# Performance work log

Measured on AMD Instinct MI355X. Metric: run time of the kernel, lower is better.

## Reference

```python
import jax, jax.numpy as jnp
import numpy as np

B, L, H, T, C = 64, 1024, 512, 100, 97


def setup_inputs() -> dict:
    key = jax.random.key(0)
    k1, k2, k3, k4, k5 = jax.random.split(key, 5)
    return {
        "position_fmap": jax.random.normal(k1, (B, L, H), dtype=jnp.float32),
        "origin_fmap": jax.random.normal(k2, (B, L, H), dtype=jnp.float32),
        "pos_emb": jax.random.normal(k3, (T, H), dtype=jnp.float32),
        "W_gen": jax.random.normal(k4, (C, H), dtype=jnp.float32) * (1.0 / np.sqrt(H)),
        "b_gen": jax.random.normal(k5, (C,), dtype=jnp.float32) * 0.01,
    }


def reference(position_fmap, origin_fmap, pos_emb, W_gen, b_gen):
    # The torch loop over t in [0, T) computes, per step, scores = fmap @ emb_t,
    # softmax over L, then context = a^T @ origin_fmap. Batched over all steps:
    scores = jnp.einsum('blh,th->btl', position_fmap, pos_emb)   # [B, T, L]
    attn = jax.nn.softmax(scores, axis=-1)                       # softmax over spatial L
    context = jnp.einsum('btl,blh->bth', attn, origin_fmap)      # [B, T, H]
    # generator: Linear(H -> num_classes)
    return jnp.einsum('bth,ch->btc', context, W_gen) + b_gen     # [B, T, C]
```

## Files before the change

### kernel.cpp

```cpp
#include <hip/hip_runtime.h>
#include <hip/hip_bf16.h>

#define B_   64
#define L_   1024
#define H_   512
#define T_   100
#define C_   97
#define TP_  112

typedef _Float16 h8 __attribute__((ext_vector_type(8)));
typedef __attribute__((ext_vector_type(4))) float f32x4;

__global__ __launch_bounds__(256) void k0_prep(
    const float* __restrict__ emb, const float* __restrict__ W,
    _Float16* __restrict__ embh, _Float16* __restrict__ Wh) {
  const int row = blockIdx.x, tid = threadIdx.x;
  if (row < TP_) {
    for (int j = tid; j < H_; j += 256)
      embh[(size_t)row * H_ + j] =
          (row < T_) ? (_Float16)emb[(size_t)row * H_ + j] : (_Float16)0.f;
  } else {
    const int c = row - TP_;
    for (int j = tid; j < H_; j += 256)
      Wh[(size_t)c * H_ + j] =
          (c < C_) ? (_Float16)W[(size_t)c * H_ + j] : (_Float16)0.f;
  }
}

__global__ __launch_bounds__(256, 4) void k1_scores(
    const float* __restrict__ fmap, const _Float16* __restrict__ embh,
    _Float16* __restrict__ scT, float* __restrict__ part) {
  __shared__ float red_m[4 * TP_];
  __shared__ float red_s[4 * TP_];
  __shared__ float sMb[TP_];
  __shared__ _Float16 tile[TP_ * 72];
  const int tid = threadIdx.x;
  const int wave = tid >> 6, lane = tid & 63;
  const int quad = lane >> 4, cc = lane & 15;
  const int b = blockIdx.x >> 4;
  const int m0 = blockIdx.x * 64 + wave * 16;

  f32x4 acc[7];
#pragma unroll
  for (int i = 0; i < 7; ++i) acc[i] = (f32x4){0.f, 0.f, 0.f, 0.f};

  const float* ap = fmap + (size_t)(m0 + cc) * H_ + quad * 8;
#pragma unroll 2
  for (int k = 0; k < H_; k += 32) {
    float4 x0 = *(const float4*)(ap + k);
    float4 x1 = *(const float4*)(ap + k + 4);
    h8 a;
    a[0] = (_Float16)x0.x; a[1] = (_Float16)x0.y;
    a[2] = (_Float16)x0.z; a[3] = (_Float16)x0.w;
    a[4] = (_Float16)x1.x; a[5] = (_Float16)x1.y;
    a[6] = (_Float16)x1.z; a[7] = (_Float16)x1.w;
#pragma unroll
    for (int i = 0; i < 7; ++i) {
      h8 bf = *(const h8*)(embh + (size_t)(i * 16 + cc) * H_ + k + quad * 8);
      acc[i] = __builtin_amdgcn_mfma_f32_16x16x32_f16(a, bf, acc[i], 0, 0, 0);
    }
  }

  float pm[7], ps[7];
#pragma unroll
  for (int i = 0; i < 7; ++i) {
    float m = acc[i][0];
#pragma unroll
    for (int r = 1; r < 4; ++r) m = fmaxf(m, acc[i][r]);
    float s = 0.f;
#pragma unroll
    for (int r = 0; r < 4; ++r) s += __expf(acc[i][r] - m);
    pm[i] = m; ps[i] = s;
  }
#pragma unroll
  for (int d = 16; d < 64; d <<= 1) {
#pragma unroll
    for (int i = 0; i < 7; ++i) {
      float om = __shfl_xor(pm[i], d, 64);
      float os = __shfl_xor(ps[i], d, 64);
      float M = fmaxf(pm[i], om);
      ps[i] = ps[i] * __expf(pm[i] - M) + os * __expf(om - M);
      pm[i] = M;
    }
  }
  if (lane < 16) {
#pragma unroll
    for (int i = 0; i < 7; ++i) {
      red_m[wave * TP_ + i * 16 + lane] = pm[i];
      red_s[wave * TP_ + i * 16 + lane] = ps[i];
    }
  }
  __syncthreads();
  if (tid < TP_) {
    float M = red_m[tid], S = red_s[tid];
#pragma unroll
    for (int w = 1; w < 4; ++w) {
      float om = red_m[w * TP_ + tid], os = red_s[w * TP_ + tid];
      float nM = fmaxf(M, om);
      S = S * __expf(M - nM) + os * __expf(om - nM);
      M = nM;
    }
    float* p = part + ((size_t)blockIdx.x * TP_ + tid) * 2;
    p[0] = M; p[1] = S;
    sMb[tid] = M;
  }
  __syncthreads();
#pragma unroll
  for (int i = 0; i < 7; ++i) {
    float mb = sMb[i * 16 + cc];
#pragma unroll
    for (int r = 0; r < 4; ++r)
      tile[(i * 16 + cc) * 72 + wave * 16 + quad * 4 + r] = (_Float16)(acc[i][r] - mb);
  }
  __syncthreads();
  _Float16* dst = scT + (size_t)b * TP_ * L_ + (size_t)(blockIdx.x & 15) * 64;
  for (int idx = tid; idx < 896; idx += 256) {
    const int t = idx >> 3, c = idx & 7;
    h8 v = *(const h8*)&tile[t * 72 + c * 8];
    *(h8*)(dst + (size_t)t * L_ + c * 8) = v;
  }
}

__global__ __launch_bounds__(256) void k2_softmax(
    const _Float16* __restrict__ scT, const float* __restrict__ part,
    _Float16* __restrict__ attnT) {
  __shared__ float sAdj[16 * 14];
  __shared__ float sInv[14];
  const int b = blockIdx.x >> 3, tg = blockIdx.x & 7;
  const int tid = threadIdx.x;
  if (tid < 14) {
    const int t = tg * 14 + tid;
    float M = -1e30f, S = 0.f;
    for (int k = 0; k < 16; ++k) {
      const float* p = part + ((size_t)(b * 16 + k) * TP_ + t) * 2;
      float om = p[0], os = p[1];
      float nM = fmaxf(M, om);
      S = S * __expf(M - nM) + os * __expf(om - nM);
      M = nM;
    }
    sInv[tid] = 1.f / S;
    for (int k = 0; k < 16; ++k)
      sAdj[k * 14 + tid] = part[((size_t)(b * 16 + k) * TP_ + t) * 2] - M;
  }
  __syncthreads();
  const size_t base = ((size_t)b * TP_ + tg * 14) * L_;
  for (int idx = tid; idx < 14 * 128; idx += 256) {
    const int t = idx >> 7, c = idx & 127;
    const size_t off = base + (size_t)t * L_ + c * 8;
    h8 v = *(const h8*)(scT + off);
    const float adj = sAdj[(c >> 3) * 14 + t];
    const float inv = sInv[t];
    h8 o;
#pragma unroll
    for (int j = 0; j < 8; ++j)
      o[j] = (_Float16)(__expf((float)v[j] + adj) * inv);
    *(h8*)(attnT + off) = o;
  }
}

__global__ __launch_bounds__(256) void k3_context(
    const _Float16* __restrict__ attnT, const float* __restrict__ origin,
    _Float16* __restrict__ ctx) {
  const int b = blockIdx.x >> 3, hb = (blockIdx.x & 7) * 64;
  const int tid = threadIdx.x;
  const int wave = tid >> 6, lane = tid & 63;
  const int quad = lane >> 4, cc = lane & 15;

  f32x4 acc[7];
#pragma unroll
  for (int i = 0; i < 7; ++i) acc[i] = (f32x4){0.f, 0.f, 0.f, 0.f};

  const _Float16* aA = attnT + ((size_t)b * TP_ + cc) * L_ + quad * 8;
  const float* bp = origin + ((size_t)b * L_ + quad * 8) * H_ + hb + wave * 16 + cc;

#pragma unroll 2
  for (int l0 = 0; l0 < L_; l0 += 32) {
    h8 bfh;
#pragma unroll
    for (int j = 0; j < 8; ++j) bfh[j] = (_Float16)bp[(size_t)(l0 + j) * H_];
#pragma unroll
    for (int i = 0; i < 7; ++i) {
      h8 af = *(const h8*)(aA + (size_t)(i * 16) * L_ + l0);
      acc[i] = __builtin_amdgcn_mfma_f32_16x16x32_f16(af, bfh, acc[i], 0, 0, 0);
    }
  }
  const int h = hb + wave * 16 + cc;
#pragma unroll
  for (int i = 0; i < 7; ++i)
#pragma unroll
    for (int r = 0; r < 4; ++r)
      ctx[((size_t)b * TP_ + i * 16 + quad * 4 + r) * H_ + h] = (_Float16)acc[i][r];
}

__global__ __launch_bounds__(256) void k4_out(
    const _Float16* __restrict__ ctx, const _Float16* __restrict__ Wh,
    const float* __restrict__ bias, float* __restrict__ out) {
  const int b = blockIdx.x / 7, mt = blockIdx.x % 7;
  const int tid = threadIdx.x;
  const int wave = tid >> 6, lane = tid & 63;
  const int quad = lane >> 4, cc = lane & 15;
  f32x4 acc0 = (f32x4){0.f, 0.f, 0.f, 0.f};
  f32x4 acc1 = (f32x4){0.f, 0.f, 0.f, 0.f};
  const int c0 = wave * 16 + cc;
  const int c1 = (wave + 4) * 16 + cc;
  const bool hasB = (wave < 3);
  const _Float16* ap  = ctx + ((size_t)b * TP_ + mt * 16 + cc) * H_ + quad * 8;
  const _Float16* b0p = Wh + (size_t)c0 * H_ + quad * 8;
  const _Float16* b1p = Wh + (size_t)(hasB ? c1 : c0) * H_ + quad * 8;
#pragma unroll 2
  for (int k = 0; k < H_; k += 32) {
    h8 af = *(const h8*)(ap + k);
    h8 bf0 = *(const h8*)(b0p + k);
    acc0 = __builtin_amdgcn_mfma_f32_16x16x32_f16(af, bf0, acc0, 0, 0, 0);
    if (hasB) {
      h8 bf1 = *(const h8*)(b1p + k);
      acc1 = __builtin_amdgcn_mfma_f32_16x16x32_f16(af, bf1, acc1, 0, 0, 0);
    }
  }
  const float bias0 = (c0 < C_) ? bias[c0] : 0.f;
  const float bias1 = (hasB && c1 < C_) ? bias[c1] : 0.f;
#pragma unroll
  for (int r = 0; r < 4; ++r) {
    const int t = mt * 16 + quad * 4 + r;
    if (t < T_) {
      if (c0 < C_) out[((size_t)b * T_ + t) * C_ + c0] = acc0[r] + bias0;
      if (hasB && c1 < C_) out[((size_t)b * T_ + t) * C_ + c1] = acc1[r] + bias1;
    }
  }
}

extern "C" void kernel_launch(void* const* d_in, const int* in_sizes, int n_in,
                              void* d_out, int out_size, void* d_ws, size_t ws_size,
                              hipStream_t stream) {
  const float* fmap   = (const float*)d_in[0];
  const float* origin = (const float*)d_in[1];
  const float* emb    = (const float*)d_in[2];
  const float* W      = (const float*)d_in[3];
  const float* bias   = (const float*)d_in[4];
  float* out = (float*)d_out;

  char* ws = (char*)d_ws;
  _Float16* embh  = (_Float16*)(ws);
  _Float16* Wh    = (_Float16*)(ws + 114688);
  _Float16* scT   = (_Float16*)(ws + 229376);
  float*    part  = (float*)   (ws + 14909440);
  _Float16* attnT = (_Float16*)(ws + 15826944);
  _Float16* ctx   = (_Float16*)(ws + 30507008);

  hipLaunchKernelGGL(k0_prep,    dim3(224),  dim3(256), 0, stream, emb, W, embh, Wh);
  hipLaunchKernelGGL(k1_scores,  dim3(1024), dim3(256), 0, stream, fmap, embh, scT, part);
  hipLaunchKernelGGL(k2_softmax, dim3(512),  dim3(256), 0, stream, scT, part, attnT);
  hipLaunchKernelGGL(k3_context, dim3(512),  dim3(256), 0, stream, attnT, origin, ctx);
  hipLaunchKernelGGL(k4_out,     dim3(448),  dim3(256), 0, stream, ctx, Wh, bias, out);
}
```

Measured before the change: 375.7 us.

## Split context GEMM over L, move score transpose into softmax, widen score blocks

The context kernel gains a 4-way split over the sequence dimension, going from 512 to 2048 blocks and writing four partial fp16 context buffers. The output kernel sums those partials before its GEMM. The scores kernel now uses 512-thread blocks covering 128 rows and writes untransposed scores straight to global memory. The softmax kernel transposes them through shared memory. The intent is better occupancy and parallelism in the heavy context GEMM, at the cost of extra partial-buffer traffic, fp16 partial-sum precision loss, and uncoalesced strided score stores.

```diff
diff --git a/kernel.cpp b/kernel.cpp
--- a/kernel.cpp
+++ b/kernel.cpp
@@ -27,25 +27,23 @@
   }
 }
 
-__global__ __launch_bounds__(256, 4) void k1_scores(
+__global__ __launch_bounds__(512, 4) void k1_scores(
     const float* __restrict__ fmap, const _Float16* __restrict__ embh,
-    _Float16* __restrict__ scT, float* __restrict__ part) {
-  __shared__ float red_m[4 * TP_];
-  __shared__ float red_s[4 * TP_];
+    _Float16* __restrict__ sc, float* __restrict__ part) {
+  __shared__ float red_m[8 * TP_];
+  __shared__ float red_s[8 * TP_];
   __shared__ float sMb[TP_];
-  __shared__ _Float16 tile[TP_ * 72];
   const int tid = threadIdx.x;
   const int wave = tid >> 6, lane = tid & 63;
   const int quad = lane >> 4, cc = lane & 15;
-  const int b = blockIdx.x >> 4;
-  const int m0 = blockIdx.x * 64 + wave * 16;
+  const int m0 = blockIdx.x * 128 + wave * 16;
 
   f32x4 acc[7];
 #pragma unroll
   for (int i = 0; i < 7; ++i) acc[i] = (f32x4){0.f, 0.f, 0.f, 0.f};
 
   const float* ap = fmap + (size_t)(m0 + cc) * H_ + quad * 8;
-#pragma unroll 2
+#pragma unroll 4
   for (int k = 0; k < H_; k += 32) {
     float4 x0 = *(const float4*)(ap + k);
     float4 x1 = *(const float4*)(ap + k + 4);
@@ -94,7 +92,7 @@
   if (tid < TP_) {
     float M = red_m[tid], S = red_s[tid];
 #pragma unroll
-    for (int w = 1; w < 4; ++w) {
+    for (int w = 1; w < 8; ++w) {
       float om = red_m[w * TP_ + tid], os = red_s[w * TP_ + tid];
       float nM = fmaxf(M, om);
       S = S * __expf(M - nM) + os * __expf(om - nM);
@@ -110,58 +108,60 @@
     float mb = sMb[i * 16 + cc];
 #pragma unroll
     for (int r = 0; r < 4; ++r)
-      tile[(i * 16 + cc) * 72 + wave * 16 + quad * 4 + r] = (_Float16)(acc[i][r] - mb);
-  }
-  __syncthreads();
-  _Float16* dst = scT + (size_t)b * TP_ * L_ + (size_t)(blockIdx.x & 15) * 64;
-  for (int idx = tid; idx < 896; idx += 256) {
-    const int t = idx >> 3, c = idx & 7;
-    h8 v = *(const h8*)&tile[t * 72 + c * 8];
-    *(h8*)(dst + (size_t)t * L_ + c * 8) = v;
+      sc[(size_t)(m0 + quad * 4 + r) * TP_ + i * 16 + cc] =
+          (_Float16)(acc[i][r] - mb);
   }
 }
 
 __global__ __launch_bounds__(256) void k2_softmax(
-    const _Float16* __restrict__ scT, const float* __restrict__ part,
+    const _Float16* __restrict__ sc, const float* __restrict__ part,
     _Float16* __restrict__ attnT) {
-  __shared__ float sAdj[16 * 14];
-  __shared__ float sInv[14];
-  const int b = blockIdx.x >> 3, tg = blockIdx.x & 7;
-  const int tid = threadIdx.x;
-  if (tid < 14) {
-    const int t = tg * 14 + tid;
+  __shared__ float sAdj[TP_], sInv[TP_];
+  __shared__ _Float16 tile[TP_ * 152];
+  const int b = blockIdx.x >> 3, ch = blockIdx.x & 7;
+  const int tid = threadIdx.x;
+  if (tid < TP_) {
     float M = -1e30f, S = 0.f;
-    for (int k = 0; k < 16; ++k) {
-      const float* p = part + ((size_t)(b * 16 + k) * TP_ + t) * 2;
+    for (int k = 0; k < 8; ++k) {
+      const float* p = part + ((size_t)(b * 8 + k) * TP_ + tid) * 2;
       float om = p[0], os = p[1];
       float nM = fmaxf(M, om);
       S = S * __expf(M - nM) + os * __expf(om - nM);
       M = nM;
     }
     sInv[tid] = 1.f / S;
-    for (int k = 0; k < 16; ++k)
-      sAdj[k * 14 + tid] = part[((size_t)(b * 16 + k) * TP_ + t) * 2] - M;
-  }
-  __syncthreads();
-  const size_t base = ((size_t)b * TP_ + tg * 14) * L_;
-  for (int idx = tid; idx < 14 * 128; idx += 256) {
-    const int t = idx >> 7, c = idx & 127;
-    const size_t off = base + (size_t)t * L_ + c * 8;
-    h8 v = *(const h8*)(scT + off);
-    const float adj = sAdj[(c >> 3) * 14 + t];
-    const float inv = sInv[t];
-    h8 o;
-#pragma unroll
-    for (int j = 0; j < 8; ++j)
-      o[j] = (_Float16)(__expf((float)v[j] + adj) * inv);
-    *(h8*)(attnT + off) = o;
-  }
-}
-
-__global__ __launch_bounds__(256) void k3_context(
+    sAdj[tid] = part[((size_t)(b * 8 + ch) * TP_ + tid) * 2] - M;
+  }
+  __syncthreads();
+  const _Float16* sp = sc + ((size_t)(b * 8 + ch) * 128) * TP_;
+#pragma unroll
+  for (int j = 0; j < 7; ++j) {
+    const int id = tid + j * 256;
+    const int l = id / 14, tc = id % 14;
+    h8 v = *(const h8*)(sp + (size_t)l * TP_ + tc * 8);
+#pragma unroll
+    for (int jj = 0; jj < 8; ++jj) {
+      const int t = tc * 8 + jj;
+      tile[t * 152 + l] = (_Float16)(__expf((float)v[jj] + sAdj[t]) * sInv[t]);
+    }
+  }
+  __syncthreads();
+  _Float16* dst = attnT + (size_t)b * TP_ * L_ + ch * 128;
+#pragma unroll
+  for (int j = 0; j < 7; ++j) {
+    const int id = tid + j * 256;
+    const int t = id >> 4, c = id & 15;
+    *(h8*)(dst + (size_t)t * L_ + c * 8) = *(const h8*)&tile[t * 152 + c * 8];
+  }
+}
+
+__global__ __launch_bounds__(256, 4) void k3_context(
     const _Float16* __restrict__ attnT, const float* __restrict__ origin,
-    _Float16* __restrict__ ctx) {
-  const int b = blockIdx.x >> 3, hb = (blockIdx.x & 7) * 64;
+    _Float16* __restrict__ ctxp) {
+  const int bid = blockIdx.x;
+  const int hb = (bid & 7) * 64;
+  const int ks = (bid >> 3) & 3;
+  const int b  = bid >> 5;
   const int tid = threadIdx.x;
   const int wave = tid >> 6, lane = tid & 63;
   const int quad = lane >> 4, cc = lane & 15;
@@ -170,11 +170,12 @@
 #pragma unroll
   for (int i = 0; i < 7; ++i) acc[i] = (f32x4){0.f, 0.f, 0.f, 0.f};
 
-  const _Float16* aA = attnT + ((size_t)b * TP_ + cc) * L_ + quad * 8;
-  const float* bp = origin + ((size_t)b * L_ + quad * 8) * H_ + hb + wave * 16 + cc;
+  const _Float16* aA = attnT + ((size_t)b * TP_ + cc) * L_ + ks * 256 + quad * 8;
+  const float* bp = origin + ((size_t)b * L_ + ks * 256 + quad * 8) * H_ +
+                    hb + wave * 16 + cc;
 
 #pragma unroll 2
-  for (int l0 = 0; l0 < L_; l0 += 32) {
+  for (int l0 = 0; l0 < 256; l0 += 32) {
     h8 bfh;
 #pragma unroll
     for (int j = 0; j < 8; ++j) bfh[j] = (_Float16)bp[(size_t)(l0 + j) * H_];
@@ -185,15 +186,16 @@
     }
   }
   const int h = hb + wave * 16 + cc;
+  _Float16* out = ctxp + ((size_t)(ks * B_ + b) * TP_) * H_;
 #pragma unroll
   for (int i = 0; i < 7; ++i)
 #pragma unroll
     for (int r = 0; r < 4; ++r)
-      ctx[((size_t)b * TP_ + i * 16 + quad * 4 + r) * H_ + h] = (_Float16)acc[i][r];
+      out[(size_t)(i * 16 + quad * 4 + r) * H_ + h] = (_Float16)acc[i][r];
 }
 
 __global__ __launch_bounds__(256) void k4_out(
-    const _Float16* __restrict__ ctx, const _Float16* __restrict__ Wh,
+    const _Float16* __restrict__ ctxp, const _Float16* __restrict__ Wh,
     const float* __restrict__ bias, float* __restrict__ out) {
   const int b = blockIdx.x / 7, mt = blockIdx.x % 7;
   const int tid = threadIdx.x;
@@ -204,12 +206,20 @@
   const int c0 = wave * 16 + cc;
   const int c1 = (wave + 4) * 16 + cc;
   const bool hasB = (wave < 3);
-  const _Float16* ap  = ctx + ((size_t)b * TP_ + mt * 16 + cc) * H_ + quad * 8;
+  const size_t arow = ((size_t)b * TP_ + mt * 16 + cc) * H_ + quad * 8;
+  const _Float16* ap0 = ctxp + arow;
+  const _Float16* ap1 = ctxp + (size_t)1 * B_ * TP_ * H_ + arow;
+  const _Float16* ap2 = ctxp + (size_t)2 * B_ * TP_ * H_ + arow;
+  const _Float16* ap3 = ctxp + (size_t)3 * B_ * TP_ * H_ + arow;
   const _Float16* b0p = Wh + (size_t)c0 * H_ + quad * 8;
   const _Float16* b1p = Wh + (size_t)(hasB ? c1 : c0) * H_ + quad * 8;
 #pragma unroll 2
   for (int k = 0; k < H_; k += 32) {
-    h8 af = *(const h8*)(ap + k);
+    h8 a0 = *(const h8*)(ap0 + k);
+    h8 a1 = *(const h8*)(ap1 + k);
+    h8 a2 = *(const h8*)(ap2 + k);
+    h8 a3 = *(const h8*)(ap3 + k);
+    h8 af = (a0 + a1) + (a2 + a3);
     h8 bf0 = *(const h8*)(b0p + k);
     acc0 = __builtin_amdgcn_mfma_f32_16x16x32_f16(af, bf0, acc0, 0, 0, 0);
     if (hasB) {
@@ -242,14 +252,14 @@
   char* ws = (char*)d_ws;
   _Float16* embh  = (_Float16*)(ws);
   _Float16* Wh    = (_Float16*)(ws + 114688);
-  _Float16* scT   = (_Float16*)(ws + 229376);
+  _Float16* sc    = (_Float16*)(ws + 229376);
   float*    part  = (float*)   (ws + 14909440);
-  _Float16* attnT = (_Float16*)(ws + 15826944);
-  _Float16* ctx   = (_Float16*)(ws + 30507008);
+  _Float16* attnT = (_Float16*)(ws + 15368192);
+  _Float16* ctxp  = (_Float16*)(ws + 30048256);
 
   hipLaunchKernelGGL(k0_prep,    dim3(224),  dim3(256), 0, stream, emb, W, embh, Wh);
-  hipLaunchKernelGGL(k1_scores,  dim3(1024), dim3(256), 0, stream, fmap, embh, scT, part);
-  hipLaunchKernelGGL(k2_softmax, dim3(512),  dim3(256), 0, stream, scT, part, attnT);
-  hipLaunchKernelGGL(k3_context, dim3(512),  dim3(256), 0, stream, attnT, origin, ctx);
-  hipLaunchKernelGGL(k4_out,     dim3(448),  dim3(256), 0, stream, ctx, Wh, bias, out);
-}
+  hipLaunchKernelGGL(k1_scores,  dim3(512),  dim3(512), 0, stream, fmap, embh, sc, part);
+  hipLaunchKernelGGL(k2_softmax, dim3(512),  dim3(256), 0, stream, sc, part, attnT);
+  hipLaunchKernelGGL(k3_context, dim3(2048), dim3(256), 0, stream, attnT, origin, ctxp);
+  hipLaunchKernelGGL(k4_out,     dim3(448),  dim3(256), 0, stream, ctxp, Wh, bias, out);
+}
```

Result: slower. 399.3 us (+6.3%).
